# Kernel tuning notes

Hardware: AMD Instinct MI355X
Metric: run time of the kernel (lower is better)

Reference implementation:

```python
import jax, jax.numpy as jnp
import numpy as np
import math

EMB_DIM = 3        # positional embedding dim of the implicit Hyena filter
FILTER_ORDER = 64  # hidden width of the implicit filter MLP


def rmsnorm(x, w, eps=1e-8):
    return x * jax.lax.rsqrt(jnp.mean(x * x, axis=-1, keepdims=True) + eps) * w


def _implicit_filter(L, D, mlp_w1, mlp_b1, freq1, mlp_w2, mlp_b2, freq2, mlp_w3):
    # positional embedding (emb_dim=3): [t, Re exp(-i f w), Im exp(-i f w)], bands=1
    t = jnp.linspace(0.0, 1.0, L)[:, None]                               # (L,1)
    w = 2.0 * math.pi * jnp.linspace(0.0, L - 1.0, L)[:, None] / L       # (L,1)
    f = jnp.linspace(1e-4, 0.0, 1)[None, :]                              # (1,1)
    ang = f * w
    z = jnp.concatenate([t, jnp.cos(ang), -jnp.sin(ang)], axis=-1)       # (L,3)
    # implicit filter MLP with Sin activations
    h = jnp.sin(freq1 * (z @ mlp_w1.T + mlp_b1))
    h = jnp.sin(freq2 * (h @ mlp_w2.T + mlp_b2))
    h = h @ mlp_w3.T                                                     # (L,D)
    # exponential modulation (modulate=True)
    fast, slow, target = 0.3, 1.5, 1e-2
    max_decay = math.log(target) / fast
    min_decay = math.log(target) / slow
    deltas = jnp.linspace(min_decay, max_decay, D)[None, :]              # (1,D)
    h = h * jnp.exp(-t * jnp.abs(deltas))
    return h.T                                                           # (D,L)


def _fftconv(v, k, bias):
    # causal long conv via zero-padded FFT. v: (B,D,L), k: (D,L), bias: (D,)
    L = v.shape[-1]
    n = 2 * L
    kf = jnp.fft.rfft(k, n=n) / n
    y = jnp.fft.irfft(jnp.fft.rfft(v, n=n) * kf, n=n, norm="forward")[..., :L]
    return y + v * bias[None, :, None]


def _block(x, norm_in_w, in_proj_w, in_proj_b, short_filter_w, short_filter_b,
           mlp_w1, mlp_b1, freq1, mlp_w2, mlp_b2, freq2, mlp_w3, filter_bias,
           out_proj_w, out_proj_b, norm_w, ffn_w1, ffn_b1, ffn_w2, ffn_b2):
    B, L, D = x.shape
    xn = rmsnorm(x, norm_in_w)
    # Hyena operator
    u = (xn @ in_proj_w.T + in_proj_b).transpose(0, 2, 1)                # (B,3D,L)
    uc = jax.lax.conv_general_dilated(
        u, short_filter_w, (1,), [(2, 0)],
        feature_group_count=3 * D, dimension_numbers=("NCH", "OIH", "NCH"))
    uc = uc + short_filter_b[None, :, None]                              # causal k=3 depthwise
    x0, x1, v = jnp.split(uc, 3, axis=1)                                 # (B,D,L) each
    k = _implicit_filter(L, D, mlp_w1, mlp_b1, freq1, mlp_w2, mlp_b2, freq2, mlp_w3)
    v = _fftconv(v * x1, k, filter_bias)                                 # gate, long conv
    y = (v * x0).transpose(0, 2, 1) @ out_proj_w.T + out_proj_b          # gate, out proj
    # residual + FFN
    h = y + x
    o = rmsnorm(h, norm_w)
    o = jax.nn.gelu(o @ ffn_w1.T + ffn_b1) @ ffn_w2.T + ffn_b2
    return o + h


def setup_inputs():
    key = jax.random.key(0)
    B, L, D = 4, 2048, 1024
    ks = jax.random.split(key, 12)

    def lin(k, out_d, in_d):
        return jax.random.normal(k, (out_d, in_d), jnp.float32) * (1.0 / math.sqrt(in_d))

    return {
        "x": jax.random.normal(ks[0], (B, L, D), jnp.float32),
        "norm_in_w": jnp.ones((D,), jnp.float32),
        "in_proj_w": lin(ks[1], 3 * D, D),
        "in_proj_b": jnp.zeros((3 * D,), jnp.float32),
        "short_filter_w": jax.random.normal(ks[2], (3 * D, 1, 3), jnp.float32) / math.sqrt(3.0),
        "short_filter_b": jnp.zeros((3 * D,), jnp.float32),
        "mlp_w1": lin(ks[3], FILTER_ORDER, EMB_DIM),
        "mlp_b1": jnp.zeros((FILTER_ORDER,), jnp.float32),
        "freq1": jnp.ones((FILTER_ORDER,), jnp.float32),
        "mlp_w2": lin(ks[4], FILTER_ORDER, FILTER_ORDER),
        "mlp_b2": jnp.zeros((FILTER_ORDER,), jnp.float32),
        "freq2": jnp.ones((FILTER_ORDER,), jnp.float32),
        "mlp_w3": lin(ks[5], D, FILTER_ORDER),
        "filter_bias": jax.random.normal(ks[6], (D,), jnp.float32),
        "out_proj_w": lin(ks[7], D, D),
        "out_proj_b": jnp.zeros((D,), jnp.float32),
        "norm_w": jnp.ones((D,), jnp.float32),
        "ffn_w1": lin(ks[8], 2 * D, D),
        "ffn_b1": jnp.zeros((2 * D,), jnp.float32),
        "ffn_w2": lin(ks[9], D, 2 * D),
        "ffn_b2": jnp.zeros((D,), jnp.float32),
    }


def reference(x, norm_in_w, in_proj_w, in_proj_b, short_filter_w, short_filter_b,
              mlp_w1, mlp_b1, freq1, mlp_w2, mlp_b2, freq2, mlp_w3, filter_bias,
              out_proj_w, out_proj_b, norm_w, ffn_w1, ffn_b1, ffn_w2, ffn_b2):
    return _block(x, norm_in_w, in_proj_w, in_proj_b, short_filter_w, short_filter_b,
                  mlp_w1, mlp_b1, freq1, mlp_w2, mlp_b2, freq2, mlp_w3, filter_bias,
                  out_proj_w, out_proj_b, norm_w, ffn_w1, ffn_b1, ffn_w2, ffn_b2)
```

## Files before the change

### kernel.cpp

```cpp
#include <hip/hip_runtime.h>
#include <hip/hip_bf16.h>
#include <cstddef>

#define BB 4
#define LL 2048
#define DD 1024
#define MM (BB*LL)
#define KF_STRIDE 2056

#define SWZ(a) ((a) ^ (((a) >> 4) & 12))

typedef __bf16 bf16_t;
typedef __attribute__((ext_vector_type(8))) __bf16 bf16x8;
typedef __attribute__((ext_vector_type(4))) __bf16 bf16x4;
typedef __attribute__((ext_vector_type(4))) float f32x4;

#define GLD_LDS16(gp, lp) __builtin_amdgcn_global_load_lds(                 \
    (const __attribute__((address_space(1))) unsigned int*)(gp),            \
    (__attribute__((address_space(3))) unsigned int*)(lp), 16, 0, 0)

__device__ __forceinline__ float gelu_tanh(float x) {
    const float c = 0.7978845608028654f;
    float t = tanhf(c * (x + 0.044715f * x * x * x));
    return 0.5f * x * (1.0f + t);
}

__device__ __forceinline__ float2 cmul(float2 a, float2 b) {
    return make_float2(a.x * b.x - a.y * b.y, a.x * b.y + a.y * b.x);
}

__global__ __launch_bounds__(256) void cast_bf16_kernel(
    const float* __restrict__ in, bf16_t* __restrict__ out)
{
    const int i = (blockIdx.x * 256 + threadIdx.x) * 4;
    const float4 v = *(const float4*)(in + i);
    bf16x4 o;
    o[0] = (bf16_t)v.x; o[1] = (bf16_t)v.y; o[2] = (bf16_t)v.z; o[3] = (bf16_t)v.w;
    *(bf16x4*)(out + i) = o;
}

__global__ __launch_bounds__(256) void rmsnorm_bf16_kernel(
    const float* __restrict__ in, const float* __restrict__ w,
    bf16_t* __restrict__ out)
{
    const int row = blockIdx.x;
    const float4* ip = (const float4*)(in + (size_t)row * DD);
    float4 v = ip[threadIdx.x];
    float ss = v.x*v.x + v.y*v.y + v.z*v.z + v.w*v.w;
    #pragma unroll
    for (int off = 32; off > 0; off >>= 1) ss += __shfl_down(ss, off, 64);
    __shared__ float sums[4];
    const int wid = threadIdx.x >> 6;
    if ((threadIdx.x & 63) == 0) sums[wid] = ss;
    __syncthreads();
    const float tot = sums[0] + sums[1] + sums[2] + sums[3];
    const float scale = rsqrtf(tot * (1.0f / (float)DD) + 1e-8f);
    const float4 wv = ((const float4*)w)[threadIdx.x];
    bf16x4 o;
    o[0] = (bf16_t)(v.x * scale * wv.x);
    o[1] = (bf16_t)(v.y * scale * wv.y);
    o[2] = (bf16_t)(v.z * scale * wv.z);
    o[3] = (bf16_t)(v.w * scale * wv.w);
    *(bf16x4*)(out + (size_t)row * DD + threadIdx.x * 4) = o;
}

template<int EPI, bool BF16OUT, bool BIASROW = false>
__global__ __launch_bounds__(256) void gemm_mfma_kernel(
    const bf16_t* __restrict__ A,
    const bf16_t* __restrict__ W,
    const float* __restrict__ bias,
    const float* __restrict__ res,
    float* __restrict__ Cf,
    bf16_t* __restrict__ Cb,
    int M, int N, int K)
{
    __shared__ __align__(16) bf16_t As[128 * 32];
    __shared__ __align__(16) bf16_t Ws[128 * 32];
    const int tid  = threadIdx.x;
    const int bm   = blockIdx.y * 128;
    const int bn   = blockIdx.x * 128;
    const int lane = tid & 63;
    const int wave = tid >> 6;
    const int wr   = (wave >> 1) * 64;
    const int wc   = (wave & 1) * 64;

    const int lrow = tid >> 2;
    const int lcol = (tid & 3) * 8;

    const bf16_t* Ag = A + (size_t)(bm + lrow) * K + lcol;
    const bf16_t* Wg = W + (size_t)(bn + lrow) * K + lcol;
    bf16_t* AsL0 = As + lrow * 32 + lcol;
    bf16_t* AsL1 = As + (64 + lrow) * 32 + lcol;
    bf16_t* WsL0 = Ws + lrow * 32 + lcol;
    bf16_t* WsL1 = Ws + (64 + lrow) * 32 + lcol;

    f32x4 acc[4][4] = {};

    const int fr = lane & 15;
    const int fc = (lane >> 4) * 8;

    for (int k0 = 0; k0 < K; k0 += 32) {
        GLD_LDS16(Ag + k0,                AsL0);
        GLD_LDS16(Ag + (size_t)64*K + k0, AsL1);
        GLD_LDS16(Wg + k0,                WsL0);
        GLD_LDS16(Wg + (size_t)64*K + k0, WsL1);
        __syncthreads();

        bf16x8 af[4], wf[4];
        #pragma unroll
        for (int i = 0; i < 4; ++i)
            af[i] = *(const bf16x8*)(As + (wr + i*16 + fr) * 32 + fc);
        #pragma unroll
        for (int j = 0; j < 4; ++j)
            wf[j] = *(const bf16x8*)(Ws + (wc + j*16 + fr) * 32 + fc);
        #pragma unroll
        for (int i = 0; i < 4; ++i)
            #pragma unroll
            for (int j = 0; j < 4; ++j)
                acc[i][j] = __builtin_amdgcn_mfma_f32_16x16x32_bf16(
                    af[i], wf[j], acc[i][j], 0, 0, 0);
        __syncthreads();
    }

    const int fq = lane >> 4;
    #pragma unroll
    for (int i = 0; i < 4; ++i) {
        const int row0 = bm + wr + i*16 + fq*4;
        #pragma unroll
        for (int j = 0; j < 4; ++j) {
            const int col = bn + wc + j*16 + fr;
            const float bcol = BIASROW ? 0.0f : bias[col];
            #pragma unroll
            for (int r = 0; r < 4; ++r) {
                float v = acc[i][j][r] + (BIASROW ? bias[row0 + r] : bcol);
                if constexpr (EPI == 2) v = gelu_tanh(v);
                if constexpr (EPI == 1) v += res[(size_t)(row0 + r) * N + col];
                if constexpr (BF16OUT)
                    Cb[(size_t)(row0 + r) * N + col] = (bf16_t)v;
                else
                    Cf[(size_t)(row0 + r) * N + col] = v;
            }
        }
    }
}

__global__ __launch_bounds__(256) void shortfilter_kernel(
    const bf16_t* __restrict__ ut, const float* __restrict__ sw,
    const float* __restrict__ sb, bf16_t* __restrict__ x0t,
    float* __restrict__ vin)
{
    const int d = blockIdx.x;
    const int c0 = d, c1 = DD + d, c2 = 2 * DD + d;
    const float w0a = sw[c0*3+0], w0b = sw[c0*3+1], w0c = sw[c0*3+2], b0 = sb[c0];
    const float w1a = sw[c1*3+0], w1b = sw[c1*3+1], w1c = sw[c1*3+2], b1 = sb[c1];
    const float w2a = sw[c2*3+0], w2b = sw[c2*3+1], w2c = sw[c2*3+2], b2 = sb[c2];
    const bf16_t* r0 = ut + (size_t)c0 * MM;
    const bf16_t* r1 = ut + (size_t)c1 * MM;
    const bf16_t* r2 = ut + (size_t)c2 * MM;
    bf16_t* o0 = x0t + (size_t)d * MM;
    float*  o1 = vin + (size_t)d * MM;
    for (int m = threadIdx.x; m < MM; m += 256) {
        const int l = m & (LL - 1);
        float v0 = w0c * (float)r0[m] + b0;
        float v1 = w1c * (float)r1[m] + b1;
        float v2 = w2c * (float)r2[m] + b2;
        if (l >= 1) {
            v0 += w0b * (float)r0[m-1];
            v1 += w1b * (float)r1[m-1];
            v2 += w2b * (float)r2[m-1];
        }
        if (l >= 2) {
            v0 += w0a * (float)r0[m-2];
            v1 += w1a * (float)r1[m-2];
            v2 += w2a * (float)r2[m-2];
        }
        o0[m] = (bf16_t)v0;
        o1[m] = v2 * v1;
    }
}

__global__ __launch_bounds__(256) void filtermlp_kernel(
    const float* __restrict__ w1, const float* __restrict__ b1,
    const float* __restrict__ f1, const float* __restrict__ w2,
    const float* __restrict__ b2, const float* __restrict__ f2,
    float* __restrict__ h2t)
{
    __shared__ float w2s[64 * 64];
    for (int i = threadIdx.x; i < 64 * 64; i += 256) w2s[i] = w2[i];
    __syncthreads();
    const int l = blockIdx.x * 256 + threadIdx.x;
    const float t = (float)l / (float)(LL - 1);
    const float ang = 1e-4f * 6.283185307179586f * (float)l / (float)LL;
    const float z0 = t, z1 = cosf(ang), z2 = -sinf(ang);
    float h1[64];
    #pragma unroll
    for (int j = 0; j < 64; ++j) {
        const float s = w1[j*3+0]*z0 + w1[j*3+1]*z1 + w1[j*3+2]*z2 + b1[j];
        h1[j] = sinf(f1[j] * s);
    }
    for (int j = 0; j < 64; ++j) {
        float s = b2[j];
        #pragma unroll
        for (int jj = 0; jj < 64; ++jj) s += w2s[j*64 + jj] * h1[jj];
        h2t[j * LL + l] = sinf(f2[j] * s);
    }
}

__global__ __launch_bounds__(256) void filtermod_kernel(
    const float* __restrict__ w3, const float* __restrict__ h2t,
    float* __restrict__ kfilt)
{
    __shared__ float w3s[32 * 64];
    const int d0 = blockIdx.y * 32;
    const int l  = blockIdx.x * 256 + threadIdx.x;
    for (int i = threadIdx.x; i < 32 * 64; i += 256) w3s[i] = w3[d0 * 64 + i];
    __syncthreads();
    float acc[32] = {};
    for (int j = 0; j < 64; ++j) {
        const float v = h2t[j * LL + l];
        #pragma unroll
        for (int dd = 0; dd < 32; ++dd) acc[dd] += w3s[dd*64 + j] * v;
    }
    const float t = (float)l / (float)(LL - 1);
    const float min_decay = -3.0701134573253944f;
    const float max_decay = -15.350567286626972f;
    #pragma unroll
    for (int dd = 0; dd < 32; ++dd) {
        const int d = d0 + dd;
        const float delta = fabsf(min_decay + (max_decay - min_decay) * (float)d / (float)(DD - 1));
        kfilt[(size_t)d * LL + l] = acc[dd] * expf(-t * delta);
    }
}

template<int SIGN>
__device__ __forceinline__ void fft4096_r4_ip(float2* __restrict__ buf)
{
    const float fsign = (float)SIGN;
    const int tid = threadIdx.x;
    #pragma unroll
    for (int t = 0; t < 6; ++t) {
        const int ls = 2 * t;
        const float theta = fsign * 6.283185307179586f / (float)(4096 >> ls);
        float2 a[2][4];
        #pragma unroll
        for (int u = 0; u < 2; ++u) {
            const int idx = tid + u * 512;
            #pragma unroll
            for (int m = 0; m < 4; ++m)
                a[u][m] = buf[SWZ(idx + m * 1024)];
        }
        __syncthreads();
        #pragma unroll
        for (int u = 0; u < 2; ++u) {
            const int idx = tid + u * 512;
            const int p = idx >> ls;
            const int q = idx & ((1 << ls) - 1);
            float sn, cs;
            __sincosf(theta * (float)p, &sn, &cs);
            const float2 W  = make_float2(cs, sn);
            const float2 W2 = make_float2(cs*cs - sn*sn, 2.0f*cs*sn);
            const float2 u0 = make_float2(a[u][0].x + a[u][2].x, a[u][0].y + a[u][2].y);
            const float2 u1 = make_float2(a[u][1].x + a[u][3].x, a[u][1].y + a[u][3].y);
            const float2 t2 = make_float2(a[u][0].x - a[u][2].x, a[u][0].y - a[u][2].y);
            const float2 t3 = make_float2(a[u][1].x - a[u][3].x, a[u][1].y - a[u][3].y);
            const float2 u2 = cmul(W, t2);
            const float2 it3 = make_float2(-fsign * t3.y, fsign * t3.x);
            const float2 u3 = cmul(W, it3);
            const int o = q + (p << (ls + 2));
            buf[SWZ(o)]             = make_float2(u0.x + u1.x, u0.y + u1.y);
            buf[SWZ(o + (1 << ls))] = make_float2(u2.x + u3.x, u2.y + u3.y);
            buf[SWZ(o + (2 << ls))] = cmul(make_float2(u0.x - u1.x, u0.y - u1.y), W2);
            buf[SWZ(o + (3 << ls))] = cmul(make_float2(u2.x - u3.x, u2.y - u3.y), W2);
        }
        __syncthreads();
    }
}

__global__ __launch_bounds__(512) void kfft_kernel(
    const float* __restrict__ kfilt, float2* __restrict__ Kf)
{
    __shared__ float2 fb[4096];
    const int d0 = blockIdx.x * 2;
    const float* k0 = kfilt + (size_t)d0 * LL;
    const float* k1 = k0 + LL;
    const float inv = 1.0f / 4096.0f;
    const int tid = threadIdx.x;
    for (int i = tid; i < 2048; i += 512) {
        fb[SWZ(i)]        = make_float2(k0[i] * inv, k1[i] * inv);
        fb[SWZ(i + 2048)] = make_float2(0.f, 0.f);
    }
    __syncthreads();
    fft4096_r4_ip<-1>(fb);
    float2* o0 = Kf + (size_t)d0 * KF_STRIDE;
    float2* o1 = o0 + KF_STRIDE;
    for (int k = tid; k <= 2048; k += 512) {
        const float2 z1 = fb[SWZ(k)];
        const float2 z2 = fb[SWZ((4096 - k) & 4095)];
        o0[k] = make_float2(0.5f * (z1.x + z2.x), 0.5f * (z1.y - z2.y));
        o1[k] = make_float2(0.5f * (z1.y + z2.y), 0.5f * (z2.x - z1.x));
    }
}

__global__ __launch_bounds__(512) void fftconv_kernel(
    float* __restrict__ vio, const float2* __restrict__ Kf,
    const float* __restrict__ fbias)
{
    __shared__ float2 fb[4096];
    const int blk = blockIdx.x;
    const int d   = blk >> 1;
    float* v1 = vio + (size_t)(2 * blk) * LL;
    float* v2 = v1 + LL;
    const int tid = threadIdx.x;
    for (int i = tid; i < 2048; i += 512) {
        fb[SWZ(i)]        = make_float2(v1[i], v2[i]);
        fb[SWZ(i + 2048)] = make_float2(0.f, 0.f);
    }
    __syncthreads();
    fft4096_r4_ip<-1>(fb);
    const float2* kf = Kf + (size_t)d * KF_STRIDE;
    for (int i = tid; i < 4096; i += 512) {
        float2 k;
        if (i <= 2048) k = kf[i];
        else { const float2 t = kf[4096 - i]; k = make_float2(t.x, -t.y); }
        fb[SWZ(i)] = cmul(fb[SWZ(i)], k);
    }
    __syncthreads();
    fft4096_r4_ip<1>(fb);
    const float bias = fbias[d];
    for (int i = tid; i < 2048; i += 512) {
        const float2 zy = fb[SWZ(i)];
        v1[i] = zy.x + bias * v1[i];
        v2[i] = zy.y + bias * v2[i];
    }
}

__global__ __launch_bounds__(256) void gate_transpose_kernel(
    const float* __restrict__ y, const bf16_t* __restrict__ x0t,
    bf16_t* __restrict__ g)
{
    __shared__ float tile[32][33];
    const int b  = blockIdx.z;
    const int l0 = blockIdx.x * 32;
    const int d0 = blockIdx.y * 32;
    const int tx  = threadIdx.x & 31;
    const int tyb = threadIdx.x >> 5;
    #pragma unroll
    for (int i = 0; i < 4; ++i) {
        const int dy = tyb + i * 8;
        const size_t src = ((size_t)(d0 + dy) * BB + b) * LL + l0 + tx;
        tile[dy][tx] = y[src] * (float)x0t[src];
    }
    __syncthreads();
    #pragma unroll
    for (int i = 0; i < 4; ++i) {
        const int ly = tyb + i * 8;
        g[((size_t)(b * LL + l0 + ly)) * DD + d0 + tx] = (bf16_t)tile[tx][ly];
    }
}

extern "C" void kernel_launch(void* const* d_in, const int* in_sizes, int n_in,
                              void* d_out, int out_size, void* d_ws, size_t ws_size,
                              hipStream_t stream)
{
    (void)in_sizes; (void)n_in; (void)out_size; (void)ws_size;
    const float* x   = (const float*)d_in[0];
    const float* nw0 = (const float*)d_in[1];
    const float* ipw = (const float*)d_in[2];
    const float* ipb = (const float*)d_in[3];
    const float* sfw = (const float*)d_in[4];
    const float* sfb = (const float*)d_in[5];
    const float* w1  = (const float*)d_in[6];
    const float* b1  = (const float*)d_in[7];
    const float* f1  = (const float*)d_in[8];
    const float* w2  = (const float*)d_in[9];
    const float* b2  = (const float*)d_in[10];
    const float* f2  = (const float*)d_in[11];
    const float* w3  = (const float*)d_in[12];
    const float* fbv = (const float*)d_in[13];
    const float* opw = (const float*)d_in[14];
    const float* opb = (const float*)d_in[15];
    const float* nw1 = (const float*)d_in[16];
    const float* fw1 = (const float*)d_in[17];
    const float* fb1 = (const float*)d_in[18];
    const float* fw2 = (const float*)d_in[19];
    const float* fb2 = (const float*)d_in[20];
    float* out = (float*)d_out;

    float* ws = (float*)d_ws;
    bf16_t* utb    = (bf16_t*)ws;
    bf16_t* gatedb = (bf16_t*)ws;
    float*  h      = ws + 4194304;
    bf16_t* midb   = (bf16_t*)(ws + 12582912);
    bf16_t* xnb    = (bf16_t*)(ws + 25165824);
    bf16_t* x0tb   = (bf16_t*)(ws + 29360128);
    float*  vio    = ws + 37748736;
    float*  kfilt  = ws + 46137344;
    float2* Kf     = (float2*)(ws + 48234496);
    bf16_t* ipwb   = (bf16_t*)(ws + 52445184);
    bf16_t* opwb   = ipwb + 3145728;
    bf16_t* fw1b   = opwb + 1048576;
    bf16_t* fw2b   = fw1b + 2097152;
    float*  h2t    = ws + 56639488;

    cast_bf16_kernel<<<3072*1024/1024, 256, 0, stream>>>(ipw, ipwb);
    cast_bf16_kernel<<<1024*1024/1024, 256, 0, stream>>>(opw, opwb);
    cast_bf16_kernel<<<2048*1024/1024, 256, 0, stream>>>(fw1, fw1b);
    cast_bf16_kernel<<<2048*1024/1024, 256, 0, stream>>>(fw2, fw2b);
    filtermlp_kernel<<<LL/256, 256, 0, stream>>>(w1, b1, f1, w2, b2, f2, h2t);
    filtermod_kernel<<<dim3(LL/256, DD/32), 256, 0, stream>>>(w3, h2t, kfilt);
    kfft_kernel<<<DD/2, 512, 0, stream>>>(kfilt, Kf);
    rmsnorm_bf16_kernel<<<MM, 256, 0, stream>>>(x, nw0, xnb);
    gemm_mfma_kernel<0, true, true><<<dim3(MM/128, 3072/128), 256, 0, stream>>>(
        ipwb, xnb, ipb, nullptr, nullptr, utb, 3*DD, MM, DD);
    shortfilter_kernel<<<DD, 256, 0, stream>>>(utb, sfw, sfb, x0tb, vio);
    fftconv_kernel<<<BB*DD/2, 512, 0, stream>>>(vio, Kf, fbv);
    gate_transpose_kernel<<<dim3(LL/32, DD/32, BB), 256, 0, stream>>>(vio, x0tb, gatedb);
    gemm_mfma_kernel<1, false><<<dim3(DD/128, MM/128), 256, 0, stream>>>(
        gatedb, opwb, opb, x, h, nullptr, MM, DD, DD);
    rmsnorm_bf16_kernel<<<MM, 256, 0, stream>>>(h, nw1, xnb);
    gemm_mfma_kernel<2, true><<<dim3(2*DD/128, MM/128), 256, 0, stream>>>(
        xnb, fw1b, fb1, nullptr, nullptr, midb, MM, 2*DD, DD);
    gemm_mfma_kernel<1, false><<<dim3(DD/128, MM/128), 256, 0, stream>>>(
        midb, fw2b, fb2, h, out, nullptr, MM, DD, 2*DD);
}
```

Measured before the change: 589.6 us.

## Switch LDS FFT to radix-8 stages and merge weight casts into one launch

Replaces the six-stage radix-4 in-place shared-memory FFT with a four-stage radix-8 FFT. Each thread now handles one 8-point butterfly per stage instead of two 4-point ones, which cuts the number of barrier-separated LDS round trips. It also adds launch_bounds occupancy hints to the FFT kernels and fuses the four weight-cast launches into a single kernel. The radix-8 butterfly raises register pressure and changes the twiddle computation, which could affect accuracy or occupancy.

Measured after the change: 581.0 us. No clear change (-1.5%).

```diff
diff --git a/kernel.cpp b/kernel.cpp
--- a/kernel.cpp
+++ b/kernel.cpp
@@ -28,15 +28,33 @@
 __device__ __forceinline__ float2 cmul(float2 a, float2 b) {
     return make_float2(a.x * b.x - a.y * b.y, a.x * b.y + a.y * b.x);
 }
-
-__global__ __launch_bounds__(256) void cast_bf16_kernel(
-    const float* __restrict__ in, bf16_t* __restrict__ out)
-{
-    const int i = (blockIdx.x * 256 + threadIdx.x) * 4;
-    const float4 v = *(const float4*)(in + i);
+__device__ __forceinline__ float2 cadd(float2 a, float2 b) {
+    return make_float2(a.x + b.x, a.y + b.y);
+}
+__device__ __forceinline__ float2 csub(float2 a, float2 b) {
+    return make_float2(a.x - b.x, a.y - b.y);
+}
+__device__ __forceinline__ float2 cmuli(float2 z, float s) {
+    return make_float2(-s * z.y, s * z.x);
+}
+
+__global__ __launch_bounds__(256) void cast_all_kernel(
+    const float* __restrict__ s0, const float* __restrict__ s1,
+    const float* __restrict__ s2, const float* __restrict__ s3,
+    bf16_t* __restrict__ d0, bf16_t* __restrict__ d1,
+    bf16_t* __restrict__ d2, bf16_t* __restrict__ d3)
+{
+    const int b = blockIdx.x;
+    const float* s; bf16_t* d; int base;
+    if (b < 3072)      { s = s0; d = d0; base = b; }
+    else if (b < 4096) { s = s1; d = d1; base = b - 3072; }
+    else if (b < 6144) { s = s2; d = d2; base = b - 4096; }
+    else               { s = s3; d = d3; base = b - 6144; }
+    const int i = (base * 256 + threadIdx.x) * 4;
+    const float4 v = *(const float4*)(s + i);
     bf16x4 o;
     o[0] = (bf16_t)v.x; o[1] = (bf16_t)v.y; o[2] = (bf16_t)v.z; o[3] = (bf16_t)v.w;
-    *(bf16x4*)(out + i) = o;
+    *(bf16x4*)(d + i) = o;
 }
 
 __global__ __launch_bounds__(256) void rmsnorm_bf16_kernel(
@@ -233,50 +251,61 @@
 }
 
 template<int SIGN>
-__device__ __forceinline__ void fft4096_r4_ip(float2* __restrict__ buf)
-{
-    const float fsign = (float)SIGN;
+__device__ __forceinline__ void fft4096_r8_ip(float2* __restrict__ buf)
+{
+    const float fs = (float)SIGN;
+    const float RH = 0.7071067811865476f;
     const int tid = threadIdx.x;
     #pragma unroll
-    for (int t = 0; t < 6; ++t) {
-        const int ls = 2 * t;
-        const float theta = fsign * 6.283185307179586f / (float)(4096 >> ls);
-        float2 a[2][4];
-        #pragma unroll
-        for (int u = 0; u < 2; ++u) {
-            const int idx = tid + u * 512;
-            #pragma unroll
-            for (int m = 0; m < 4; ++m)
-                a[u][m] = buf[SWZ(idx + m * 1024)];
-        }
+    for (int t = 0; t < 4; ++t) {
+        const int ls = 3 * t;
+        const int s  = 1 << ls;
+        const float theta = fs * 6.283185307179586f / (float)(4096 >> ls);
+        float2 a[8];
+        #pragma unroll
+        for (int m = 0; m < 8; ++m) a[m] = buf[SWZ(tid + m * 512)];
         __syncthreads();
-        #pragma unroll
-        for (int u = 0; u < 2; ++u) {
-            const int idx = tid + u * 512;
-            const int p = idx >> ls;
-            const int q = idx & ((1 << ls) - 1);
-            float sn, cs;
-            __sincosf(theta * (float)p, &sn, &cs);
-            const float2 W  = make_float2(cs, sn);
-            const float2 W2 = make_float2(cs*cs - sn*sn, 2.0f*cs*sn);
-            const float2 u0 = make_float2(a[u][0].x + a[u][2].x, a[u][0].y + a[u][2].y);
-            const float2 u1 = make_float2(a[u][1].x + a[u][3].x, a[u][1].y + a[u][3].y);
-            const float2 t2 = make_float2(a[u][0].x - a[u][2].x, a[u][0].y - a[u][2].y);
-            const float2 t3 = make_float2(a[u][1].x - a[u][3].x, a[u][1].y - a[u][3].y);
-            const float2 u2 = cmul(W, t2);
-            const float2 it3 = make_float2(-fsign * t3.y, fsign * t3.x);
-            const float2 u3 = cmul(W, it3);
-            const int o = q + (p << (ls + 2));
-            buf[SWZ(o)]             = make_float2(u0.x + u1.x, u0.y + u1.y);
-            buf[SWZ(o + (1 << ls))] = make_float2(u2.x + u3.x, u2.y + u3.y);
-            buf[SWZ(o + (2 << ls))] = cmul(make_float2(u0.x - u1.x, u0.y - u1.y), W2);
-            buf[SWZ(o + (3 << ls))] = cmul(make_float2(u2.x - u3.x, u2.y - u3.y), W2);
-        }
+        const int p = tid >> ls;
+        const int q = tid & (s - 1);
+        float sn, cs;
+        __sincosf(theta * (float)p, &sn, &cs);
+        const float2 W1 = make_float2(cs, sn);
+        const float2 W2 = cmul(W1, W1);
+        const float2 W3 = cmul(W2, W1);
+        const float2 W4 = cmul(W2, W2);
+        const float2 W5 = cmul(W4, W1);
+        const float2 W6 = cmul(W4, W2);
+        const float2 W7 = cmul(W4, W3);
+        const float2 es = cadd(a[0], a[4]), ed = csub(a[0], a[4]);
+        const float2 fs2 = cadd(a[2], a[6]), fd = csub(a[2], a[6]);
+        const float2 E0 = cadd(es, fs2);
+        const float2 E1 = cadd(ed, cmuli(fd, fs));
+        const float2 E2 = csub(es, fs2);
+        const float2 E3 = csub(ed, cmuli(fd, fs));
+        const float2 os = cadd(a[1], a[5]), od = csub(a[1], a[5]);
+        const float2 gs = cadd(a[3], a[7]), gd = csub(a[3], a[7]);
+        const float2 O0 = cadd(os, gs);
+        const float2 O1 = cadd(od, cmuli(gd, fs));
+        const float2 O2 = csub(os, gs);
+        const float2 O3 = csub(od, cmuli(gd, fs));
+        const float2 T0 = O0;
+        const float2 T1 = make_float2(RH * (O1.x - fs * O1.y), RH * (fs * O1.x + O1.y));
+        const float2 T2 = cmuli(O2, fs);
+        const float2 T3 = make_float2(RH * (-O3.x - fs * O3.y), RH * (fs * O3.x - O3.y));
+        const int o = q + (p << (ls + 3));
+        buf[SWZ(o)]         = cadd(E0, T0);
+        buf[SWZ(o + s)]     = cmul(W1, cadd(E1, T1));
+        buf[SWZ(o + 2*s)]   = cmul(W2, cadd(E2, T2));
+        buf[SWZ(o + 3*s)]   = cmul(W3, cadd(E3, T3));
+        buf[SWZ(o + 4*s)]   = cmul(W4, csub(E0, T0));
+        buf[SWZ(o + 5*s)]   = cmul(W5, csub(E1, T1));
+        buf[SWZ(o + 6*s)]   = cmul(W6, csub(E2, T2));
+        buf[SWZ(o + 7*s)]   = cmul(W7, csub(E3, T3));
         __syncthreads();
     }
 }
 
-__global__ __launch_bounds__(512) void kfft_kernel(
+__global__ __launch_bounds__(512, 4) void kfft_kernel(
     const float* __restrict__ kfilt, float2* __restrict__ Kf)
 {
     __shared__ float2 fb[4096];
@@ -290,7 +319,7 @@
         fb[SWZ(i + 2048)] = make_float2(0.f, 0.f);
     }
     __syncthreads();
-    fft4096_r4_ip<-1>(fb);
+    fft4096_r8_ip<-1>(fb);
     float2* o0 = Kf + (size_t)d0 * KF_STRIDE;
     float2* o1 = o0 + KF_STRIDE;
     for (int k = tid; k <= 2048; k += 512) {
@@ -301,7 +330,7 @@
     }
 }
 
-__global__ __launch_bounds__(512) void fftconv_kernel(
+__global__ __launch_bounds__(512, 4) void fftconv_kernel(
     float* __restrict__ vio, const float2* __restrict__ Kf,
     const float* __restrict__ fbias)
 {
@@ -316,7 +345,7 @@
         fb[SWZ(i + 2048)] = make_float2(0.f, 0.f);
     }
     __syncthreads();
-    fft4096_r4_ip<-1>(fb);
+    fft4096_r8_ip<-1>(fb);
     const float2* kf = Kf + (size_t)d * KF_STRIDE;
     for (int i = tid; i < 4096; i += 512) {
         float2 k;
@@ -325,7 +354,7 @@
         fb[SWZ(i)] = cmul(fb[SWZ(i)], k);
     }
     __syncthreads();
-    fft4096_r4_ip<1>(fb);
+    fft4096_r8_ip<1>(fb);
     const float bias = fbias[d];
     for (int i = tid; i < 2048; i += 512) {
         const float2 zy = fb[SWZ(i)];
@@ -402,10 +431,8 @@
     bf16_t* fw2b   = fw1b + 2097152;
     float*  h2t    = ws + 56639488;
 
-    cast_bf16_kernel<<<3072*1024/1024, 256, 0, stream>>>(ipw, ipwb);
-    cast_bf16_kernel<<<1024*1024/1024, 256, 0, stream>>>(opw, opwb);
-    cast_bf16_kernel<<<2048*1024/1024, 256, 0, stream>>>(fw1, fw1b);
-    cast_bf16_kernel<<<2048*1024/1024, 256, 0, stream>>>(fw2, fw2b);
+    cast_all_kernel<<<8192, 256, 0, stream>>>(ipw, opw, fw1, fw2,
+                                              ipwb, opwb, fw1b, fw2b);
     filtermlp_kernel<<<LL/256, 256, 0, stream>>>(w1, b1, f1, w2, b2, f2, h2t);
     filtermod_kernel<<<dim3(LL/256, DD/32), 256, 0, stream>>>(w3, h2t, kfilt);
     kfft_kernel<<<DD/2, 512, 0, stream>>>(kfilt, Kf);
```
